# Kernel optimization log

Hardware: AMD Instinct MI355X
Metric: run time of the kernel (lower is better)

Reference implementation:

```python
import jax, jax.numpy as jnp
import numpy as np

B, N, DIM = 2, 2048, 2048
H, DK, DV = 16, 64, 128
DIM_INNER = (DK + DV) * H  # 3072
EPS = 1e-12  # matches F.normalize clamp_min eps


def l2norm(t):
    n = jnp.linalg.norm(t, axis=-1, keepdims=True)
    return t / jnp.maximum(n, EPS)


def tanh_norm(t):
    n = jnp.linalg.norm(t, axis=-1, keepdims=True)
    return jnp.tanh(n) * (t / jnp.maximum(n, EPS))


def setup_inputs() -> dict:
    key = jax.random.key(0)
    k1, k2, k3, k4 = jax.random.split(key, 4)
    tokens = jax.random.normal(k1, (B, N, DIM), dtype=jnp.float32)
    # Linear weights stored as [in, out] (y = x @ W)
    Wqg = jax.random.normal(k2, (DIM, DIM_INNER), dtype=jnp.float32) * (DIM ** -0.5)
    Wkv = jax.random.normal(k3, (DIM, DIM_INNER), dtype=jnp.float32) * (DIM ** -0.5)
    Wo = jax.random.normal(k4, (DV * H, DIM), dtype=jnp.float32) * ((DV * H) ** -0.5)
    # LearnedScale log_scales, init log(1.0) = 0
    ls_iaw = jnp.zeros((H,), dtype=jnp.float32)  # inverse_acceptance_width (bias=1.0)
    ls_hws = jnp.zeros((H,), dtype=jnp.float32)  # head_wise_scale (bias=0.0)
    return {"tokens": tokens, "Wqg": Wqg, "Wkv": Wkv, "Wo": Wo,
            "ls_iaw": ls_iaw, "ls_hws": ls_hws}


def _split_heads(t):
    # [b, n, h*d] -> [b, h, n, d]
    b, n, _ = t.shape
    return t.reshape(b, n, H, -1).transpose(0, 2, 1, 3)


def reference(tokens, Wqg, Wkv, Wo, ls_iaw, ls_hws):
    qg = _split_heads(tokens @ Wqg)   # [b, h, n, dk+dv]
    kv = _split_heads(tokens @ Wkv)
    queries, gates = qg[..., :DK], qg[..., DK:]
    keys, values = kv[..., :DK], kv[..., DK:]
    queries, keys, values = l2norm(queries), l2norm(keys), l2norm(values)

    sim = jnp.einsum('bhid,bhjd->bhij', queries, keys)
    # r = 1 / (exp(log_scales) + 1)  (LearnedScale bias=1.0)
    r = 1.0 / (jnp.exp(ls_iaw) + 1.0)[None, :, None, None]
    attn = jnp.square(jax.nn.relu(1.0 - r * (1.0 - sim)))
    # NOTE: original code applies causal mask to `sim` AFTER computing `attn`,
    # so the mask has no effect on the output -- replicated faithfully here.
    aggr = jnp.einsum('bhij,bhjd->bhid', attn, values)
    out = tanh_norm(aggr) * jnp.tanh(jax.nn.silu(gates))
    out = out * jnp.exp(ls_hws)[None, :, None, None]  # head_wise_scale, bias=0
    out = out.transpose(0, 2, 1, 3).reshape(tokens.shape[0], tokens.shape[1], H * DV)
    return out @ Wo
```

## Files before the change

### kernel.cpp

```cpp
#include <hip/hip_runtime.h>
#include <hip/hip_bf16.h>
#include <stdint.h>


typedef unsigned short u16;
typedef __bf16 bf16x8 __attribute__((ext_vector_type(8)));
typedef u16 u16x8 __attribute__((ext_vector_type(8)));
typedef float f32x4 __attribute__((ext_vector_type(4)));
typedef float f32x16 __attribute__((ext_vector_type(16)));
typedef int i32x4 __attribute__((ext_vector_type(4)));

#define DEVINL __device__ __forceinline__

DEVINL u16 f2bf(float f) {
  union { float f; uint32_t u; } v; v.f = f;
  uint32_t r = (v.u + 0x7FFFu + ((v.u >> 16) & 1u)) >> 16;
  return (u16)r;
}
DEVINL float bf2f(u16 x) {
  union { uint32_t u; float f; } v; v.u = ((uint32_t)x) << 16;
  return v.f;
}
DEVINL bf16x8 as_bf(u16x8 v) { return __builtin_bit_cast(bf16x8, v); }

typedef const __attribute__((address_space(1))) uint32_t* gptr_t;
typedef __attribute__((address_space(3))) uint32_t* lptr_t;
DEVINL void gload_lds16(const void* g, void* l) {
  __builtin_amdgcn_global_load_lds((gptr_t)g, (lptr_t)l, 16, 0, 0);
}

DEVINL f32x4 mfma16(u16x8 a, u16x8 b, f32x4 c) {
  return __builtin_amdgcn_mfma_f32_16x16x32_bf16(as_bf(a), as_bf(b), c, 0, 0, 0);
}
DEVINL f32x16 mfma32(u16x8 a, u16x8 b, f32x16 c) {
  return __builtin_amdgcn_mfma_f32_32x32x16_bf16(as_bf(a), as_bf(b), c, 0, 0, 0);
}

__global__ void k_cvt(const float* __restrict__ src, u16* __restrict__ dst, int n) {
  int i = (blockIdx.x * blockDim.x + threadIdx.x) * 4;
  int stride = gridDim.x * blockDim.x * 4;
  for (; i < n; i += stride) {
    float4 f = *(const float4*)(src + i);
    ushort4 o;
    o.x = f2bf(f.x); o.y = f2bf(f.y); o.z = f2bf(f.z); o.w = f2bf(f.w);
    *(ushort4*)(dst + i) = o;
  }
}

__global__ void k_cvtT(const float* __restrict__ src, u16* __restrict__ dst, int R, int C) {
  __shared__ float tile[32][33];
  int c0 = blockIdx.x * 32, r0 = blockIdx.y * 32;
  int tc = threadIdx.x & 31, tr = threadIdx.x >> 5;
#pragma unroll
  for (int i = 0; i < 4; i++) {
    int r = tr + i * 8;
    tile[r][tc] = src[(size_t)(r0 + r) * C + c0 + tc];
  }
  __syncthreads();
#pragma unroll
  for (int i = 0; i < 4; i++) {
    int r = tr + i * 8;
    dst[(size_t)(c0 + r) * R + r0 + tc] = f2bf(tile[tc][r]);
  }
}

template <int NI, int F32OUT>
__global__ __launch_bounds__(512, 1) void k_gemmU(const u16* __restrict__ A,
                                                  const u16* __restrict__ Bt,
                                                  void* __restrict__ Cout,
                                                  int Nt, int K) {
  constexpr int BN = NI * 128;
  constexpr int NLB = BN / 64;
  constexpr int ABUF = 128 * 64;
  constexpr int BBUF = BN * 64;
  extern __shared__ char smem[];
  u16* As = (u16*)smem;
  u16* Bs = (u16*)(smem + 2 * ABUF * 2);

  const int tid = threadIdx.x, lane = tid & 63, wid = tid >> 6;

  const int NPN = Nt / BN;
  const int bid = blockIdx.x;
  const int xcd = bid & 7, idx = bid >> 3;
  const int npx = NPN >> 3;
  const int m0 = (idx & 31) * 128;
  const int n0 = (xcd * npx + (idx >> 5)) * BN;

  const int mq = (wid >> 2) * 32, nq = (wid & 3) * (BN / 8);
  const int fr = lane & 15, hi = lane >> 4, frow = hi * 4, rb7 = fr & 7;

  f32x4 acc[2][2][2][NI] = {};

  const int schunk = ((lane & 7) ^ ((lane >> 3) & 7)) << 3;
  const int srow = wid * 8 + (lane >> 3);
  const u16* ga0 = A + (size_t)(m0 + srow) * K + schunk;
  const u16* gb0 = Bt + (size_t)(n0 + srow) * K + schunk;
  const size_t l64 = (size_t)64 * K;
  const int dwave = wid * 512;

#define STG(T, P)                                                                     \
  {                                                                                   \
    const int kt_ = (T) << 6;                                                         \
    _Pragma("unroll") for (int i = 0; i < 2; i++)                                     \
        gload_lds16(ga0 + (size_t)i * l64 + kt_, As + (P) * ABUF + i * 4096 + dwave); \
    _Pragma("unroll") for (int i = 0; i < NLB; i++)                                   \
        gload_lds16(gb0 + (size_t)i * l64 + kt_, Bs + (P) * BBUF + i * 4096 + dwave); \
  }

  STG(0, 0);

  const int NTI = K >> 6;
  for (int t = 0; t < NTI; t++) {
    asm volatile("s_waitcnt vmcnt(0) lgkmcnt(0)" ::: "memory");
    __builtin_amdgcn_s_barrier();
    asm volatile("" ::: "memory");

    const int p = t & 1;
    if (t + 1 < NTI) STG(t + 1, p ^ 1);

    const u16* Ab = As + p * ABUF;
    const u16* Bb = Bs + p * BBUF;

    u16x8 af[2][2][2], bf[2][NI][2];
#pragma unroll
    for (int MH = 0; MH < 2; MH++)
#pragma unroll
      for (int mi = 0; mi < 2; mi++)
#pragma unroll
        for (int kk = 0; kk < 2; kk++) {
          const int row = MH * 64 + mq + mi * 16 + fr;
          af[MH][mi][kk] = *(const u16x8*)(Ab + row * 64 + (((kk * 4 + hi) ^ rb7) << 3));
        }
#pragma unroll
    for (int NH = 0; NH < 2; NH++)
#pragma unroll
      for (int ni = 0; ni < NI; ni++)
#pragma unroll
        for (int kk = 0; kk < 2; kk++) {
          const int row = NH * (BN / 2) + nq + ni * 16 + fr;
          bf[NH][ni][kk] = *(const u16x8*)(Bb + row * 64 + (((kk * 4 + hi) ^ rb7) << 3));
        }

    __builtin_amdgcn_s_setprio(1);
#pragma unroll
    for (int kk = 0; kk < 2; kk++)
#pragma unroll
      for (int MH = 0; MH < 2; MH++)
#pragma unroll
        for (int mi = 0; mi < 2; mi++)
#pragma unroll
          for (int NH = 0; NH < 2; NH++)
#pragma unroll
            for (int ni = 0; ni < NI; ni++)
              acc[MH][mi][NH][ni] = mfma16(af[MH][mi][kk], bf[NH][ni][kk], acc[MH][mi][NH][ni]);
    __builtin_amdgcn_s_setprio(0);
  }
#undef STG

#pragma unroll
  for (int MH = 0; MH < 2; MH++)
#pragma unroll
    for (int mi = 0; mi < 2; mi++)
#pragma unroll
      for (int NH = 0; NH < 2; NH++)
#pragma unroll
        for (int ni = 0; ni < NI; ni++)
#pragma unroll
          for (int j = 0; j < 4; j++) {
            const size_t row = m0 + MH * 64 + mq + mi * 16 + frow + j;
            const size_t col = n0 + NH * (BN / 2) + nq + ni * 16 + fr;
            if (F32OUT) ((float*)Cout)[row * Nt + col] = acc[MH][mi][NH][ni][j];
            else ((u16*)Cout)[row * Nt + col] = f2bf(acc[MH][mi][NH][ni][j]);
          }
}

__global__ __launch_bounds__(256, 4) void k_norm(const u16* __restrict__ qgkv,
                                                 u16* __restrict__ qn, u16* __restrict__ kn,
                                                 u16* __restrict__ vnT, u16* __restrict__ gact) {
  __shared__ u16 vt[128 * 64];
  const int tid = threadIdx.x, lane = tid & 63, wid = tid >> 6;
  const int hb = blockIdx.y;
  const int h = hb & 15, b = hb >> 4;
  const int n0 = blockIdx.x * 64;

  for (int s = 0; s < 16; s++) {
    const int nl = wid * 16 + s;
    const int n = n0 + nl;
    const size_t bn = (size_t)b * 2048 + n;
    const size_t baseq = bn * 6144 + (size_t)h * 192;
    const size_t basek = baseq + 3072;

    float q = bf2f(qgkv[baseq + lane]);
    float g0 = bf2f(qgkv[baseq + 64 + lane]);
    float g1 = bf2f(qgkv[baseq + 128 + lane]);
    float k = bf2f(qgkv[basek + lane]);
    float v0 = bf2f(qgkv[basek + 64 + lane]);
    float v1 = bf2f(qgkv[basek + 128 + lane]);

    float qs = q * q, ks = k * k, vs = v0 * v0 + v1 * v1;
#pragma unroll
    for (int m = 1; m < 64; m <<= 1) {
      qs += __shfl_xor(qs, m);
      ks += __shfl_xor(ks, m);
      vs += __shfl_xor(vs, m);
    }
    float rq = 1.f / fmaxf(sqrtf(qs), 1e-12f);
    float rk = 1.f / fmaxf(sqrtf(ks), 1e-12f);
    float rv = 1.f / fmaxf(sqrtf(vs), 1e-12f);

    qn[((size_t)hb * 2048 + n) * 64 + lane] = f2bf(q * rq);
    kn[((size_t)hb * 2048 + n) * 64 + lane] = f2bf(k * rk);
    float s0 = g0 / (1.f + __expf(-g0));
    float s1 = g1 / (1.f + __expf(-g1));
    gact[((size_t)hb * 2048 + n) * 128 + lane] = f2bf(tanhf(s0));
    gact[((size_t)hb * 2048 + n) * 128 + 64 + lane] = f2bf(tanhf(s1));

    const int d0 = lane, d1 = 64 + lane;
    vt[d0 * 64 + (nl ^ ((d0 & 15) << 2))] = f2bf(v0 * rv);
    vt[d1 * 64 + (nl ^ ((d1 & 15) << 2))] = f2bf(v1 * rv);
  }
  __syncthreads();

#pragma unroll
  for (int p = 0; p < 8; p++) {
    const int d = p * 16 + (tid >> 4);
    const int nq = (tid & 15) * 4;
    const int cb = nq ^ ((d & 15) << 2);
    const int nq2 = (nq & ~12) | ((nq & 4) << 1) | ((nq & 8) >> 1);
    ushort4 o;
    o.x = vt[d * 64 + cb + 0];
    o.y = vt[d * 64 + cb + 1];
    o.z = vt[d * 64 + cb + 2];
    o.w = vt[d * 64 + cb + 3];
    *(ushort4*)(vnT + ((size_t)hb * 128 + d) * 2048 + n0 + nq2) = o;
  }
}

__global__ __launch_bounds__(256, 2) void k_attn(const u16* __restrict__ qn,
                                                 const u16* __restrict__ kn,
                                                 const u16* __restrict__ vnT,
                                                 const u16* __restrict__ gact,
                                                 const float* __restrict__ ls_iaw,
                                                 const float* __restrict__ ls_hws,
                                                 u16* __restrict__ pre_out) {
  extern __shared__ char smem[];
  u16* KsB = (u16*)smem;
  u16* VsB = (u16*)(smem + 16384);
  u16* Os = (u16*)smem;

  const int tid = threadIdx.x, lane = tid & 63, wid = tid >> 6;
  const int bid = blockIdx.y * 16 + blockIdx.x;
  const int bh = (bid & 7) * 4 + ((bid >> 3) & 3);
  const int n0 = (bid >> 5) * 128;
  const int h = bh & 15;
  const int l31 = lane & 31, L = lane >> 5, rb = l31 & 7;
  const float r = 1.f / (__expf(ls_iaw[h]) + 1.f);
  const float c1 = 1.f - r;
  const float whs = __expf(ls_hws[h]);

  const int wq = wid * 32;
  const u16* qrow = qn + ((size_t)bh * 2048 + n0 + wq + l31) * 64;
  u16x8 qf[4];
#pragma unroll
  for (int c = 0; c < 4; c++) qf[c] = *(const u16x8*)(qrow + c * 16 + L * 8);

  f32x16 acc[4] = {};
  const u16* kbase = kn + (size_t)bh * 2048 * 64;
  const u16* vbase = vnT + (size_t)bh * 128 * 2048;

  int ks_goff[2];
#pragma unroll
  for (int i = 0; i < 2; i++) {
    int row = wid * 16 + i * 8 + (lane >> 3);
    ks_goff[i] = row * 64 + (((lane & 7) ^ (row & 7)) << 3);
  }
  int vs_goff[4];
#pragma unroll
  for (int i = 0; i < 4; i++) {
    int row = wid * 32 + i * 8 + (lane >> 3);
    vs_goff[i] = row * 2048 + (((lane & 7) ^ (row & 7)) << 3);
  }

  {
    u16* KsC = KsB + wid * 1024;
    u16* VsC = VsB + wid * 2048;
#pragma unroll
    for (int i = 0; i < 2; i++) gload_lds16(kbase + ks_goff[i], KsC + i * 512);
#pragma unroll
    for (int i = 0; i < 4; i++) gload_lds16(vbase + vs_goff[i], VsC + i * 512);
  }

  int cur = 0;
  for (int t = 0; t < 32; t++) {
    asm volatile("s_waitcnt vmcnt(0) lgkmcnt(0)" ::: "memory");
    __builtin_amdgcn_s_barrier();
    asm volatile("" ::: "memory");

    if (t < 31) {
      const int kv0 = (t + 1) * 64;
      u16* KsC2 = KsB + (cur ^ 1) * 4096 + wid * 1024;
      u16* VsC2 = VsB + (cur ^ 1) * 8192 + wid * 2048;
#pragma unroll
      for (int i = 0; i < 2; i++) gload_lds16(kbase + (size_t)kv0 * 64 + ks_goff[i], KsC2 + i * 512);
#pragma unroll
      for (int i = 0; i < 4; i++) gload_lds16(vbase + (size_t)vs_goff[i] + kv0, VsC2 + i * 512);
    }

    const u16* KsC = KsB + cur * 4096;
    const u16* VsC = VsB + cur * 8192;

    f32x16 sT0 = {}, sT1 = {};
    __builtin_amdgcn_s_setprio(1);
#pragma unroll
    for (int c = 0; c < 4; c++) {
      u16x8 kf0 = *(const u16x8*)(KsC + (0 + l31) * 64 + (((2 * c + L) ^ rb) << 3));
      u16x8 kf1 = *(const u16x8*)(KsC + (32 + l31) * 64 + (((2 * c + L) ^ rb) << 3));
      sT0 = mfma32(kf0, qf[c], sT0);
      sT1 = mfma32(kf1, qf[c], sT1);
    }
    __builtin_amdgcn_s_setprio(0);

    uint32_t w[2][4][2];
#pragma unroll
    for (int m = 0; m < 4; m++)
#pragma unroll
      for (int p = 0; p < 2; p++) {
        float a0 = fmaxf(0.f, fmaf(r, sT0[4 * m + 2 * p], c1));
        float a1 = fmaxf(0.f, fmaf(r, sT0[4 * m + 2 * p + 1], c1));
        float b0 = fmaxf(0.f, fmaf(r, sT1[4 * m + 2 * p], c1));
        float b1 = fmaxf(0.f, fmaf(r, sT1[4 * m + 2 * p + 1], c1));
        w[0][m][p] = (uint32_t)f2bf(a0 * a0) | ((uint32_t)f2bf(a1 * a1) << 16);
        w[1][m][p] = (uint32_t)f2bf(b0 * b0) | ((uint32_t)f2bf(b1 * b1) << 16);
      }

    __builtin_amdgcn_s_setprio(1);
#pragma unroll
    for (int kt = 0; kt < 2; kt++)
#pragma unroll
      for (int pair = 0; pair < 2; pair++) {
        i32x4 pw;
        pw[0] = (int)w[kt][2 * pair][0];
        pw[1] = (int)w[kt][2 * pair][1];
        pw[2] = (int)w[kt][2 * pair + 1][0];
        pw[3] = (int)w[kt][2 * pair + 1][1];
        u16x8 pf = __builtin_bit_cast(u16x8, pw);
        const int chunk = 4 * kt + 2 * pair + L;
#pragma unroll
        for (int dt = 0; dt < 4; dt++) {
          u16x8 vf = *(const u16x8*)(VsC + (dt * 32 + l31) * 64 + ((chunk ^ rb) << 3));
          acc[dt] = mfma32(vf, pf, acc[dt]);
        }
      }
    __builtin_amdgcn_s_setprio(0);
    cur ^= 1;
  }

  float ss = 0.f;
#pragma unroll
  for (int dt = 0; dt < 4; dt++)
#pragma unroll
    for (int e = 0; e < 16; e++) { float x = acc[dt][e]; ss += x * x; }
  ss += __shfl_xor(ss, 32);
  float nn = sqrtf(ss);
  float scale = tanhf(nn) / fmaxf(nn, 1e-12f) * whs;

  __syncthreads();

  const int q = wq + l31;
  const size_t grow = ((size_t)bh * 2048 + n0 + q) * 128;
#pragma unroll
  for (int dt = 0; dt < 4; dt++)
#pragma unroll
    for (int m = 0; m < 4; m++) {
      const int d = dt * 32 + 8 * m + 4 * L;
      ushort4 gv = *(const ushort4*)(gact + grow + d);
      ushort4 o;
      o.x = f2bf(acc[dt][4 * m + 0] * scale * bf2f(gv.x));
      o.y = f2bf(acc[dt][4 * m + 1] * scale * bf2f(gv.y));
      o.z = f2bf(acc[dt][4 * m + 2] * scale * bf2f(gv.z));
      o.w = f2bf(acc[dt][4 * m + 3] * scale * bf2f(gv.w));
      *(ushort4*)(Os + q * 132 + d) = o;
    }
  __syncthreads();

  const int orow = tid >> 1, oc0 = (tid & 1) * 64;
  const size_t obase = ((size_t)(bh >> 4) * 2048 + n0 + orow) * 2048 + (size_t)h * 128 + oc0;
#pragma unroll
  for (int j = 0; j < 16; j++) {
    ushort4 v = *(const ushort4*)(Os + orow * 132 + oc0 + 4 * j);
    *(ushort4*)(pre_out + obase + 4 * j) = v;
  }
}

extern "C" void kernel_launch(void* const* d_in, const int* in_sizes, int n_in,
                              void* d_out, int out_size, void* d_ws, size_t ws_size,
                              hipStream_t stream) {
  (void)in_sizes; (void)n_in; (void)out_size; (void)ws_size;
  const float* tokens = (const float*)d_in[0];
  const float* Wqg = (const float*)d_in[1];
  const float* Wkv = (const float*)d_in[2];
  const float* Wo = (const float*)d_in[3];
  const float* ls_iaw = (const float*)d_in[4];
  const float* ls_hws = (const float*)d_in[5];
  float* out = (float*)d_out;
  char* ws = (char*)d_ws;

  u16* WoT = (u16*)(ws + 0);
  char* regA = ws + 8388608;
  u16* tok_bf = (u16*)(regA);
  u16* WqgkvT = (u16*)(regA + 16777216);
  u16* qn = (u16*)(regA);
  u16* kn = (u16*)(regA + 8388608);
  u16* vnT = (u16*)(regA + 16777216);
  u16* gact = (u16*)(regA + 33554432);
  char* regB = ws + 58720256;
  u16* qgkv_raw = (u16*)(regB);
  u16* pre_out = (u16*)(regB);

  k_cvt<<<4096, 256, 0, stream>>>(tokens, tok_bf, 8388608);
  k_cvtT<<<dim3(96, 64), 256, 0, stream>>>(Wqg, WqgkvT, 2048, 3072);
  k_cvtT<<<dim3(96, 64), 256, 0, stream>>>(Wkv, WqgkvT + (size_t)3072 * 2048, 2048, 3072);
  k_cvtT<<<dim3(64, 64), 256, 0, stream>>>(Wo, WoT, 2048, 2048);

  k_gemmU<3, 0><<<512, 512, 131072, stream>>>(tok_bf, WqgkvT, qgkv_raw, 6144, 2048);

  k_norm<<<dim3(32, 32), 256, 0, stream>>>(qgkv_raw, qn, kn, vnT, gact);

  k_attn<<<dim3(16, 32), 256, 49152, stream>>>(qn, kn, vnT, gact, ls_iaw, ls_hws, pre_out);

  k_gemmU<2, 1><<<256, 512, 98304, stream>>>(pre_out, WoT, out, 2048, 2048);
}
```

Before: 272.3 us.

## Replace QKV projection GEMM with 256x384-tile triple-buffered kernel

Adds a dedicated GEMM for the fused Wqg/Wkv projection. It uses 256x384 output tiles, a 3-stage LDS ring with K-step 32, and a 2-wave-row by 4-wave-col layout. Global-to-LDS loads for stage t+2 are interleaved between two MFMA halves, with priority raised during the MFMA bursts. Tiles are assigned to XCDs so blocks on one XCD share B columns. The goal is higher arithmetic intensity per tile and better overlap of memory and compute than the generic kernel. The cost is a large register footprint (192 accumulators per thread) and only 256 blocks.

```diff
diff --git a/kernel.cpp b/kernel.cpp
--- a/kernel.cpp
+++ b/kernel.cpp
@@ -62,6 +62,108 @@
     int r = tr + i * 8;
     dst[(size_t)(c0 + r) * R + r0 + tc] = f2bf(tile[tc][r]);
   }
+}
+
+__global__ __launch_bounds__(512, 1) void k_gemmP2(const u16* __restrict__ A,
+                                                   const u16* __restrict__ Bt,
+                                                   u16* __restrict__ C,
+                                                   int Nt, int K) {
+  extern __shared__ char smem[];
+  u16* As = (u16*)smem;
+  u16* Bs = (u16*)(smem + 49152);
+
+  const int tid = threadIdx.x, lane = tid & 63, wid = tid >> 6;
+
+  const int bid = blockIdx.x;
+  const int xcd = bid & 7, idx = bid >> 3;
+  const int m0 = (idx & 15) * 256;
+  const int n0 = (xcd * 2 + (idx >> 4)) * 384;
+
+  const int wm = (wid >> 2) * 128, wn = (wid & 3) * 96;
+  const int fr = lane & 15, hi = lane >> 4, frow = hi * 4;
+  const int kg = (fr >> 1) & 3;
+
+  f32x4 acc[2][4][6] = {};
+
+  const int sg = ((lane & 3) ^ ((lane >> 3) & 3)) << 3;
+  const int srow = wid * 16 + (lane >> 2);
+  const u16* gA0 = A + (size_t)(m0 + srow) * K + sg;
+  const u16* gB0 = Bt + (size_t)(n0 + srow) * K + sg;
+  const size_t r128 = (size_t)128 * K;
+  const int dwave = wid * 512;
+
+#define SA(S, I, KT) gload_lds16(gA0 + (size_t)(I) * r128 + (KT), As + (S) * 8192 + (I) * 4096 + dwave)
+#define SB(S, I, KT) gload_lds16(gB0 + (size_t)(I) * r128 + (KT), Bs + (S) * 12288 + (I) * 4096 + dwave)
+
+  SA(0, 0, 0); SA(0, 1, 0); SB(0, 0, 0); SB(0, 1, 0); SB(0, 2, 0);
+  SA(1, 0, 32); SA(1, 1, 32); SB(1, 0, 32); SB(1, 1, 32); SB(1, 2, 32);
+
+  const int NTI = K >> 5;
+  int s = 0;
+  for (int t = 0; t < NTI; t++) {
+    const int s2 = (s + 2 >= 3) ? s - 1 : s + 2;
+    const int ktn = (t + 2) << 5;
+    const bool do_stage = (t + 2) < NTI;
+
+    if (t < NTI - 1) {
+      asm volatile("s_waitcnt vmcnt(5)" ::: "memory");
+    } else {
+      asm volatile("s_waitcnt vmcnt(0)" ::: "memory");
+    }
+    __builtin_amdgcn_s_barrier();
+    asm volatile("" ::: "memory");
+
+    const u16* Ab = As + s * 8192;
+    const u16* Bb = Bs + s * 12288;
+
+    u16x8 bf[6];
+#pragma unroll
+    for (int nj = 0; nj < 6; nj++)
+      bf[nj] = *(const u16x8*)(Bb + (wn + nj * 16 + fr) * 32 + ((hi ^ kg) << 3));
+    u16x8 af[4];
+#pragma unroll
+    for (int mi = 0; mi < 4; mi++)
+      af[mi] = *(const u16x8*)(Ab + (wm + mi * 16 + fr) * 32 + ((hi ^ kg) << 3));
+    if (do_stage) { SA(s2, 0, ktn); SA(s2, 1, ktn); SB(s2, 0, ktn); }
+    __builtin_amdgcn_s_setprio(1);
+#pragma unroll
+    for (int mi = 0; mi < 4; mi++)
+#pragma unroll
+      for (int nj = 0; nj < 6; nj++)
+        acc[0][mi][nj] = mfma16(af[mi], bf[nj], acc[0][mi][nj]);
+    __builtin_amdgcn_s_setprio(0);
+
+    __builtin_amdgcn_s_barrier();
+    asm volatile("" ::: "memory");
+#pragma unroll
+    for (int mi = 0; mi < 4; mi++)
+      af[mi] = *(const u16x8*)(Ab + (wm + 64 + mi * 16 + fr) * 32 + ((hi ^ kg) << 3));
+    if (do_stage) { SB(s2, 1, ktn); SB(s2, 2, ktn); }
+    __builtin_amdgcn_s_setprio(1);
+#pragma unroll
+    for (int mi = 0; mi < 4; mi++)
+#pragma unroll
+      for (int nj = 0; nj < 6; nj++)
+        acc[1][mi][nj] = mfma16(af[mi], bf[nj], acc[1][mi][nj]);
+    __builtin_amdgcn_s_setprio(0);
+
+    s = (s + 1 >= 3) ? 0 : s + 1;
+  }
+#undef SA
+#undef SB
+
+#pragma unroll
+  for (int mh = 0; mh < 2; mh++)
+#pragma unroll
+    for (int mi = 0; mi < 4; mi++)
+#pragma unroll
+      for (int nj = 0; nj < 6; nj++)
+#pragma unroll
+        for (int j = 0; j < 4; j++) {
+          const size_t row = m0 + wm + mh * 64 + mi * 16 + frow + j;
+          const size_t col = n0 + wn + nj * 16 + fr;
+          C[row * Nt + col] = f2bf(acc[mh][mi][nj][j]);
+        }
 }
 
 template <int NI, int F32OUT>
@@ -422,7 +524,7 @@
   k_cvtT<<<dim3(96, 64), 256, 0, stream>>>(Wkv, WqgkvT + (size_t)3072 * 2048, 2048, 3072);
   k_cvtT<<<dim3(64, 64), 256, 0, stream>>>(Wo, WoT, 2048, 2048);
 
-  k_gemmU<3, 0><<<512, 512, 131072, stream>>>(tok_bf, WqgkvT, qgkv_raw, 6144, 2048);
+  k_gemmP2<<<256, 512, 122880, stream>>>(tok_bf, WqgkvT, qgkv_raw, 6144, 2048);
 
   k_norm<<<dim3(32, 32), 256, 0, stream>>>(qgkv_raw, qn, kn, vnT, gact);
 
```

After: 261.4 us. -4.0%, faster.
